# Optimization experiments

Measured on AMD Instinct MI355X. Metric: run time of the kernel, lower is better.

## Reference

```python
import jax, jax.numpy as jnp
import numpy as np

NUM_HEADS = 12
LN_EPS = 1e-12


def setup_inputs() -> dict:
    key = jax.random.key(0)
    ks = jax.random.split(key, 18)
    B, S, H, I, P, KW = 8, 128, 768, 3072, 50, 100
    s = 0.02
    inp = {
        'hidden_state': jax.random.normal(ks[0], (B, S, H), jnp.float32),
        'positive_keywords': jax.random.normal(ks[1], (P, H), jnp.float32),
        'negative_keywords': jax.random.normal(ks[2], (P, H), jnp.float32),
        'attention_mask': jnp.zeros((B, 1, 1, S), jnp.float32),
        # Bilinear weights: out = (x @ W) * keyword
        'Wq': jax.random.normal(ks[3], (H, H), jnp.float32) * s,
        'Wk': jax.random.normal(ks[4], (H, H), jnp.float32) * s,
        'Wv': jax.random.normal(ks[5], (H, H), jnp.float32) * s,
        'Wo': jax.random.normal(ks[6], (H, H), jnp.float32) * s,
        'bo': jnp.zeros((H,), jnp.float32),
        # mlp: Linear(kwcount, 1)
        'Wmlp': jax.random.normal(ks[7], (KW,), jnp.float32) * s,
        'bmlp': jnp.zeros((), jnp.float32),
        # Bottleneck FFN
        'Wdown': jax.random.normal(ks[8], (H, I), jnp.float32) * s,
        'bdown': jnp.zeros((I,), jnp.float32),
        'Wup': jax.random.normal(ks[9], (I, H), jnp.float32) * s,
        'bup': jnp.zeros((H,), jnp.float32),
        'gamma': jnp.ones((H,), jnp.float32),
        'beta': jnp.zeros((H,), jnp.float32),
    }
    return inp


def reference(hidden_state, positive_keywords, negative_keywords, attention_mask,
              Wq, Wk, Wv, Wo, bo, Wmlp, bmlp, Wdown, bdown, Wup, bup, gamma, beta):
    B, S, H = hidden_state.shape
    nh = NUM_HEADS
    hd = H // nh
    # interleave pos/neg keywords -> pool [KW, H] (diff == 0, no padding)
    pool = jnp.stack((positive_keywords, negative_keywords), axis=1).reshape(-1, H)

    # shared sequence projections (keyword modulates elementwise afterwards)
    PQ = hidden_state @ Wq  # [B,S,H]
    PK = hidden_state @ Wk
    PV = hidden_state @ Wv
    scale = 1.0 / jnp.sqrt(jnp.float32(hd))

    def per_kw(kw):  # kw: [H]
        def heads(P):
            return (P * kw).reshape(B, S, nh, hd).transpose(0, 2, 1, 3)  # [B,nh,S,hd]
        Q, K, V = heads(PQ), heads(PK), heads(PV)
        scores = jnp.einsum('bhqd,bhkd->bhqk', Q, K) * scale + attention_mask
        # NOTE: softmax over dim=-2 (query axis), faithful to the original
        w = jax.nn.softmax(scores, axis=-2)
        ctx = jnp.einsum('bhqk,bhkd->bhqd', w, V)
        ctx = ctx.transpose(0, 2, 1, 3).reshape(B, S, H)
        return ctx @ Wo + bo  # [B,S,H]

    stacked = jax.vmap(per_kw)(pool)  # [KW,B,S,H]
    # mlp Linear(KW,1) over the stacked keyword axis
    fused = jnp.einsum('kbsh,k->bsh', stacked, Wmlp) + bmlp  # [B,S,H]

    # Bottleneck FFN + residual LayerNorm (dropout = identity in eval)
    down = jax.nn.gelu(fused @ Wdown + bdown, approximate=False)
    up = down @ Wup + bup
    x = up + fused
    mu = jnp.mean(x, axis=-1, keepdims=True)
    var = jnp.var(x, axis=-1, keepdims=True)
    return gamma * (x - mu) / jnp.sqrt(var + LN_EPS) + beta
```

## Files before the change

### kernel.cpp

```cpp
#include <hip/hip_runtime.h>
#include <hip/hip_bf16.h>
#include <math.h>

#define B_ 8
#define S_ 128
#define H_ 768
#define NH_ 12
#define HD_ 64
#define M_ 1024
#define KW_ 100
#define I_ 3072
#define QKVN 2304
#define NCHUNK 10
#define KWPER 10
#define LOG2E 1.4426950408889634f

typedef __attribute__((ext_vector_type(8))) short short8;
typedef __attribute__((ext_vector_type(8))) unsigned short ushort8;
typedef __attribute__((ext_vector_type(4))) float f32x4;

static __device__ __forceinline__ unsigned short f2b(float f) {
  union { float f; unsigned int u; } v; v.f = f;
  return (unsigned short)((v.u + 0x7fffu + ((v.u >> 16) & 1u)) >> 16);
}
static __device__ __forceinline__ float b2f(unsigned short b) {
  union { unsigned int u; float f; } v; v.u = ((unsigned int)b) << 16;
  return v.f;
}

__global__ void k_prep(const float* __restrict__ hidden,
                       const float* __restrict__ Wq, const float* __restrict__ Wk,
                       const float* __restrict__ Wv, const float* __restrict__ Wo,
                       const float* __restrict__ Wdown, const float* __restrict__ Wup,
                       const float* __restrict__ posk, const float* __restrict__ negk,
                       const float* __restrict__ Wmlp, const float* __restrict__ bmlp,
                       const float* __restrict__ bo,
                       unsigned short* __restrict__ hb, unsigned short* __restrict__ qkvT,
                       unsigned short* __restrict__ WoT, unsigned short* __restrict__ WdownT,
                       unsigned short* __restrict__ WupT,
                       float* __restrict__ kw2s, float* __restrict__ kwm, float* __restrict__ c0) {
  __shared__ float tile[32][33];
  int z = blockIdx.z;
  int t = threadIdx.x;
  if (z == 6) {
    int n = blockIdx.y * 96 + blockIdx.x;
    if (n < 768) {
      int i = (n * 256 + t) * 4;
      float4 v = *(const float4*)&hidden[i];
      uint2 o;
      o.x = (unsigned)f2b(v.x) | ((unsigned)f2b(v.y) << 16);
      o.y = (unsigned)f2b(v.z) | ((unsigned)f2b(v.w) << 16);
      *(uint2*)&hb[i] = o;
    } else if (n < 1068) {
      int idx = (n - 768) * 256 + t;
      if (idx < KW_ * H_) {
        int j = idx / H_, d = idx - j * H_;
        float v = (j & 1) ? negk[(j >> 1) * H_ + d] : posk[(j >> 1) * H_ + d];
        kw2s[idx] = v * v * 0.125f * LOG2E;
        kwm[idx] = v * Wmlp[j];
      }
    } else if (n == 1068) {
      __shared__ float red[256];
      red[t] = (t < KW_) ? Wmlp[t] : 0.f;
      __syncthreads();
      for (int s = 128; s > 0; s >>= 1) { if (t < s) red[t] += red[t + s]; __syncthreads(); }
      float sWm = red[0];
      for (int c = t; c < H_; c += 256) c0[c] = sWm * bo[c] + bmlp[0];
    }
    return;
  }
  const float* src; unsigned short* dst; int R, C, r0, c0t;
  if (z < 4) {
    if (blockIdx.x >= 24) return;
    const float* srcs[4] = {Wq, Wk, Wv, Wo};
    src = srcs[z];
    dst = (z < 3) ? qkvT + (size_t)z * 768 * 768 : WoT;
    R = 768; C = 768; c0t = blockIdx.x * 32; r0 = blockIdx.y * 32;
  } else if (z == 4) {
    src = Wdown; dst = WdownT; R = 768; C = 3072;
    c0t = blockIdx.x * 32; r0 = blockIdx.y * 32;
  } else {
    src = Wup; dst = WupT; R = 3072; C = 768;
    c0t = blockIdx.y * 32; r0 = blockIdx.x * 32;
  }
  int tx = t & 31, ty = t >> 5;
#pragma unroll
  for (int i = 0; i < 4; i++)
    tile[ty + i * 8][tx] = src[(size_t)(r0 + ty + i * 8) * C + c0t + tx];
  __syncthreads();
#pragma unroll
  for (int i = 0; i < 4; i++)
    dst[(size_t)(c0t + ty + i * 8) * R + r0 + tx] = f2b(tile[tx][ty + i * 8]);
}

template <int EPI>
__launch_bounds__(256)
__global__ void k_gemm_bt(const unsigned short* __restrict__ A, const unsigned short* __restrict__ BT,
                          int M, int N, int K,
                          float* __restrict__ outF, unsigned short* __restrict__ outB,
                          const float* __restrict__ bias, const float* __restrict__ res) {
  __shared__ unsigned short Asm[128][56];
  __shared__ unsigned short Bsm[128][56];
  int tid = threadIdx.x;
  int lane = tid & 63, wid = tid >> 6;
  int g = lane >> 4, c16 = lane & 15;
  int wr = wid >> 1, wc = wid & 1;
  int m0 = blockIdx.y * 128, n0 = blockIdx.x * 128;
  f32x4 acc[4][4] = {};
  int r = tid >> 1, half = (tid & 1) * 16;
  const unsigned short* Ap = A + (size_t)(m0 + r) * K + half;
  const unsigned short* Bp = BT + (size_t)(n0 + r) * K + half;
  for (int kt = 0; kt < K; kt += 32) {
    __syncthreads();
    ushort8 a0 = *(const ushort8*)(Ap + kt);
    ushort8 a1 = *(const ushort8*)(Ap + kt + 8);
    ushort8 b0 = *(const ushort8*)(Bp + kt);
    ushort8 b1 = *(const ushort8*)(Bp + kt + 8);
    *(ushort8*)&Asm[r][half] = a0;  *(ushort8*)&Asm[r][half + 8] = a1;
    *(ushort8*)&Bsm[r][half] = b0;  *(ushort8*)&Bsm[r][half + 8] = b1;
    __syncthreads();
    short8 af[4], bf[4];
#pragma unroll
    for (int mi = 0; mi < 4; mi++) af[mi] = *(const short8*)&Asm[wr * 64 + mi * 16 + c16][g * 8];
#pragma unroll
    for (int ni = 0; ni < 4; ni++) bf[ni] = *(const short8*)&Bsm[wc * 64 + ni * 16 + c16][g * 8];
#pragma unroll
    for (int mi = 0; mi < 4; mi++)
#pragma unroll
      for (int ni = 0; ni < 4; ni++)
        acc[mi][ni] = __builtin_amdgcn_mfma_f32_16x16x32_bf16(af[mi], bf[ni], acc[mi][ni], 0, 0, 0);
  }
#pragma unroll
  for (int mi = 0; mi < 4; mi++)
#pragma unroll
    for (int ni = 0; ni < 4; ni++)
#pragma unroll
      for (int rr = 0; rr < 4; rr++) {
        int row = m0 + wr * 64 + mi * 16 + g * 4 + rr;
        int col = n0 + wc * 64 + ni * 16 + c16;
        float v = acc[mi][ni][rr];
        if (EPI == 0) {
          outB[(size_t)row * N + col] = f2b(v);
        } else if (EPI == 2) {
          float t = v + bias[col];
          float gl = 0.5f * t * (1.f + erff(t * 0.70710678118f));
          outB[(size_t)row * N + col] = f2b(gl);
        }
      }
}

__launch_bounds__(256)
__global__ void k_gemm_sk(const unsigned short* __restrict__ A, const unsigned short* __restrict__ BT,
                          int M, int N, int K, int ksl, float* __restrict__ pOut) {
  __shared__ unsigned short Asm[128][56];
  __shared__ unsigned short Bsm[128][56];
  int tid = threadIdx.x;
  int lane = tid & 63, wid = tid >> 6;
  int g = lane >> 4, c16 = lane & 15;
  int wr = wid >> 1, wc = wid & 1;
  int m0 = blockIdx.y * 128, n0 = blockIdx.x * 128;
  int kstart = blockIdx.z * ksl;
  f32x4 acc[4][4] = {};
  int r = tid >> 1, half = (tid & 1) * 16;
  const unsigned short* Ap = A + (size_t)(m0 + r) * K + half + kstart;
  const unsigned short* Bp = BT + (size_t)(n0 + r) * K + half + kstart;
  for (int kt = 0; kt < ksl; kt += 32) {
    __syncthreads();
    ushort8 a0 = *(const ushort8*)(Ap + kt);
    ushort8 a1 = *(const ushort8*)(Ap + kt + 8);
    ushort8 b0 = *(const ushort8*)(Bp + kt);
    ushort8 b1 = *(const ushort8*)(Bp + kt + 8);
    *(ushort8*)&Asm[r][half] = a0;  *(ushort8*)&Asm[r][half + 8] = a1;
    *(ushort8*)&Bsm[r][half] = b0;  *(ushort8*)&Bsm[r][half + 8] = b1;
    __syncthreads();
    short8 af[4], bf[4];
#pragma unroll
    for (int mi = 0; mi < 4; mi++) af[mi] = *(const short8*)&Asm[wr * 64 + mi * 16 + c16][g * 8];
#pragma unroll
    for (int ni = 0; ni < 4; ni++) bf[ni] = *(const short8*)&Bsm[wc * 64 + ni * 16 + c16][g * 8];
#pragma unroll
    for (int mi = 0; mi < 4; mi++)
#pragma unroll
      for (int ni = 0; ni < 4; ni++)
        acc[mi][ni] = __builtin_amdgcn_mfma_f32_16x16x32_bf16(af[mi], bf[ni], acc[mi][ni], 0, 0, 0);
  }
  float* dst = pOut + (size_t)blockIdx.z * M * N;
#pragma unroll
  for (int mi = 0; mi < 4; mi++)
#pragma unroll
    for (int ni = 0; ni < 4; ni++)
#pragma unroll
      for (int rr = 0; rr < 4; rr++) {
        int row = m0 + wr * 64 + mi * 16 + g * 4 + rr;
        int col = n0 + wc * 64 + ni * 16 + c16;
        dst[(size_t)row * N + col] = acc[mi][ni][rr];
      }
}

template <int SPLITS, int EPI>
__global__ void k_red(const float* __restrict__ p, const float* __restrict__ bias,
                      float* __restrict__ outF, unsigned short* __restrict__ outB, int N) {
  int i = (blockIdx.x * 256 + threadIdx.x) * 4;
  const size_t MN = (size_t)M_ * N;
  float4 s = *(const float4*)&p[i];
#pragma unroll
  for (int c = 1; c < SPLITS; c++) {
    float4 v = *(const float4*)&p[c * MN + i];
    s.x += v.x; s.y += v.y; s.z += v.z; s.w += v.w;
  }
  if (EPI == 1) {
    int col = i % N;
    s.x += bias[col]; s.y += bias[col + 1]; s.z += bias[col + 2]; s.w += bias[col + 3];
    *(float4*)&outF[i] = s;
  }
  uint2 o;
  o.x = (unsigned)f2b(s.x) | ((unsigned)f2b(s.y) << 16);
  o.y = (unsigned)f2b(s.z) | ((unsigned)f2b(s.w) << 16);
  *(uint2*)&outB[i] = o;
}


static __device__ __forceinline__ int swzA(int r, int c) {
  return (((r << 7) + (c << 1)) ^ ((r & 7) << 4)) >> 1;
}

__launch_bounds__(512, 2)
__global__ void k_attn(const unsigned short* __restrict__ PQKV,
                       const float* __restrict__ kw2s, const float* __restrict__ kwm,
                       float* __restrict__ partial) {
  __shared__ unsigned short Ks[128 * 64];
  __shared__ unsigned short PVT[64][136];
  __shared__ unsigned short WL[8][16 * 128];
  __shared__ float SUMS[8][128];
  __shared__ float RINV[128];
  __shared__ float kw2L[KWPER * 64];
  __shared__ float kwmL[KWPER * 64];
  int tid = threadIdx.x;
  int lane = tid & 63, wid = tid >> 6;
  int g = lane >> 4, c16 = lane & 15;
  int chunk = blockIdx.x, h = blockIdx.y, b = blockIdx.z;
  const size_t rowbase = (size_t)b * 128 * QKVN;
  int kq = tid >> 2, quarter = tid & 3;
  {
    const unsigned short* srck = PQKV + rowbase + (size_t)kq * QKVN + H_ + h * HD_ + quarter * 16;
    ushort8 v0 = *(const ushort8*)srck;
    ushort8 v1 = *(const ushort8*)(srck + 8);
    *(ushort8*)&Ks[swzA(kq, quarter * 16)] = v0;
    *(ushort8*)&Ks[swzA(kq, quarter * 16 + 8)] = v1;
    const unsigned short* srcv = PQKV + rowbase + (size_t)kq * QKVN + 2 * H_ + h * HD_ + quarter * 16;
    ushort8 w0 = *(const ushort8*)srcv;
    ushort8 w1 = *(const ushort8*)(srcv + 8);
#pragma unroll
    for (int j = 0; j < 8; j++) PVT[quarter * 16 + j][kq] = w0[j];
#pragma unroll
    for (int j = 0; j < 8; j++) PVT[quarter * 16 + 8 + j][kq] = w1[j];
    for (int i = tid; i < KWPER * 64; i += 512) {
      int ki = i >> 6, d = i & 63;
      size_t gi = (size_t)(chunk * KWPER + ki) * H_ + h * HD_ + d;
      kw2L[i] = kw2s[gi];
      kwmL[i] = kwm[gi];
    }
  }
  const unsigned short* qp = PQKV + rowbase + (size_t)(wid * 16 + c16) * QKVN + h * HD_;
  ushort8 qf0 = *(const ushort8*)(qp + g * 8);
  ushort8 qf1 = *(const ushort8*)(qp + 32 + g * 8);
  __syncthreads();
  short8 kf[8][2];
#pragma unroll
  for (int t = 0; t < 8; t++)
#pragma unroll
    for (int s = 0; s < 2; s++)
      kf[t][s] = *(const short8*)&Ks[swzA(t * 16 + c16, s * 32 + g * 8)];
  short8 vf[4][4];
#pragma unroll
  for (int dt = 0; dt < 4; dt++)
#pragma unroll
    for (int s = 0; s < 4; s++)
      vf[dt][s] = *(const short8*)&PVT[dt * 16 + c16][s * 32 + g * 8];
  char* wbuf = (char*)&WL[wid][0];
  float accO[4][4] = {};
  for (int ki = 0; ki < KWPER; ki++) {
    const float* kp = &kw2L[ki * 64];
    short8 aA0, aA1;
    {
      float4 ka = *(const float4*)&kp[g * 8];
      float4 kb = *(const float4*)&kp[g * 8 + 4];
      float4 kc = *(const float4*)&kp[32 + g * 8];
      float4 kd = *(const float4*)&kp[32 + g * 8 + 4];
      union { unsigned u[4]; short8 v; } p0, p1;
      asm("v_cvt_pk_bf16_f32 %0, %1, %2" : "=v"(p0.u[0]) : "v"(b2f(qf0[0]) * ka.x), "v"(b2f(qf0[1]) * ka.y));
      asm("v_cvt_pk_bf16_f32 %0, %1, %2" : "=v"(p0.u[1]) : "v"(b2f(qf0[2]) * ka.z), "v"(b2f(qf0[3]) * ka.w));
      asm("v_cvt_pk_bf16_f32 %0, %1, %2" : "=v"(p0.u[2]) : "v"(b2f(qf0[4]) * kb.x), "v"(b2f(qf0[5]) * kb.y));
      asm("v_cvt_pk_bf16_f32 %0, %1, %2" : "=v"(p0.u[3]) : "v"(b2f(qf0[6]) * kb.z), "v"(b2f(qf0[7]) * kb.w));
      asm("v_cvt_pk_bf16_f32 %0, %1, %2" : "=v"(p1.u[0]) : "v"(b2f(qf1[0]) * kc.x), "v"(b2f(qf1[1]) * kc.y));
      asm("v_cvt_pk_bf16_f32 %0, %1, %2" : "=v"(p1.u[1]) : "v"(b2f(qf1[2]) * kc.z), "v"(b2f(qf1[3]) * kc.w));
      asm("v_cvt_pk_bf16_f32 %0, %1, %2" : "=v"(p1.u[2]) : "v"(b2f(qf1[4]) * kd.x), "v"(b2f(qf1[5]) * kd.y));
      asm("v_cvt_pk_bf16_f32 %0, %1, %2" : "=v"(p1.u[3]) : "v"(b2f(qf1[6]) * kd.z), "v"(b2f(qf1[7]) * kd.w));
      aA0 = p0.v; aA1 = p1.v;
    }
    unsigned e[8][2];
    float s8v[8];
    __builtin_amdgcn_s_setprio(1);
#pragma unroll
    for (int t = 0; t < 8; t++) {
      f32x4 z = {0.f, 0.f, 0.f, 0.f};
      z = __builtin_amdgcn_mfma_f32_16x16x32_bf16(aA0, kf[t][0], z, 0, 0, 0);
      z = __builtin_amdgcn_mfma_f32_16x16x32_bf16(aA1, kf[t][1], z, 0, 0, 0);
      float e0 = __builtin_amdgcn_exp2f(z[0]);
      float e1 = __builtin_amdgcn_exp2f(z[1]);
      float e2 = __builtin_amdgcn_exp2f(z[2]);
      float e3 = __builtin_amdgcn_exp2f(z[3]);
      s8v[t] = (e0 + e1) + (e2 + e3);
      asm("v_cvt_pk_bf16_f32 %0, %1, %2" : "=v"(e[t][0]) : "v"(e0), "v"(e1));
      asm("v_cvt_pk_bf16_f32 %0, %1, %2" : "=v"(e[t][1]) : "v"(e2), "v"(e3));
    }
    __builtin_amdgcn_s_setprio(0);
#pragma unroll
    for (int t = 0; t < 8; t++) {
      s8v[t] += __shfl_xor(s8v[t], 16);
      s8v[t] += __shfl_xor(s8v[t], 32);
    }
    if (g == 0) {
#pragma unroll
      for (int t = 0; t < 8; t++) SUMS[wid][c16 + 16 * t] = s8v[t];
    }
    __syncthreads();
    if (tid < 128) {
      float tot = 0.f;
#pragma unroll
      for (int w = 0; w < 8; w++) tot += SUMS[w][tid];
      RINV[tid] = 1.0f / tot;
    }
    __syncthreads();
    {
      int cb2 = c16 * 2;
      int qb = g * 4;
      int xb = (g & 1) * 4;
#pragma unroll
      for (int t = 0; t < 8; t++) {
        float ri = RINV[c16 + 16 * t];
        float w0 = b2f((unsigned short)(e[t][0] & 0xffffu)) * ri;
        float w1 = b2f((unsigned short)(e[t][0] >> 16)) * ri;
        float w2 = b2f((unsigned short)(e[t][1] & 0xffffu)) * ri;
        float w3 = b2f((unsigned short)(e[t][1] >> 16)) * ri;
        unsigned p01, p23;
        asm("v_cvt_pk_bf16_f32 %0, %1, %2" : "=v"(p01) : "v"(w0), "v"(w1));
        asm("v_cvt_pk_bf16_f32 %0, %1, %2" : "=v"(p23) : "v"(w2), "v"(w3));
        int tb = t * 32 + cb2;
        int a0 = ((qb + 0) * 256 + tb) ^ ((xb + 0) << 4);
        int a1 = ((qb + 1) * 256 + tb) ^ ((xb + 1) << 4);
        int a2 = ((qb + 2) * 256 + tb) ^ ((xb + 2) << 4);
        int a3 = ((qb + 3) * 256 + tb) ^ ((xb + 3) << 4);
        *(unsigned short*)(wbuf + a0) = (unsigned short)(p01 & 0xffffu);
        *(unsigned short*)(wbuf + a1) = (unsigned short)(p01 >> 16);
        *(unsigned short*)(wbuf + a2) = (unsigned short)(p23 & 0xffffu);
        *(unsigned short*)(wbuf + a3) = (unsigned short)(p23 >> 16);
      }
    }
    short8 wf[4];
#pragma unroll
    for (int s = 0; s < 4; s++)
      wf[s] = *(const short8*)(wbuf + ((c16 * 256 + s * 64 + g * 16) ^ ((c16 & 7) << 4)));
    __builtin_amdgcn_s_setprio(1);
    f32x4 zz[4];
#pragma unroll
    for (int dt = 0; dt < 4; dt++) {
      f32x4 z = {0.f, 0.f, 0.f, 0.f};
#pragma unroll
      for (int s = 0; s < 4; s++)
        z = __builtin_amdgcn_mfma_f32_16x16x32_bf16(wf[s], vf[dt][s], z, 0, 0, 0);
      zz[dt] = z;
    }
    __builtin_amdgcn_s_setprio(0);
#pragma unroll
    for (int dt = 0; dt < 4; dt++) {
      float km = kwmL[ki * 64 + dt * 16 + c16];
#pragma unroll
      for (int rr = 0; rr < 4; rr++) accO[dt][rr] += zz[dt][rr] * km;
    }
  }
  float* dst = partial + (size_t)chunk * M_ * H_;
#pragma unroll
  for (int dt = 0; dt < 4; dt++)
#pragma unroll
    for (int rr = 0; rr < 4; rr++) {
      int q = wid * 16 + g * 4 + rr;
      dst[(size_t)(b * 128 + q) * H_ + h * HD_ + dt * 16 + c16] = accO[dt][rr];
    }
}

__global__ void k_reduce(const float* __restrict__ partial, unsigned short* __restrict__ ctxsum) {
  int i = (blockIdx.x * 256 + threadIdx.x) * 4;
  float4 s = *(const float4*)&partial[i];
#pragma unroll
  for (int c = 1; c < NCHUNK; c++) {
    float4 v = *(const float4*)&partial[(size_t)c * M_ * H_ + i];
    s.x += v.x; s.y += v.y; s.z += v.z; s.w += v.w;
  }
  uint2 o;
  o.x = (unsigned)f2b(s.x) | ((unsigned)f2b(s.y) << 16);
  o.y = (unsigned)f2b(s.z) | ((unsigned)f2b(s.w) << 16);
  *(uint2*)&ctxsum[i] = o;
}

__launch_bounds__(256)
__global__ void k_ln2(const float* __restrict__ pUp, const float* __restrict__ bup,
                      const float* __restrict__ fusedF,
                      const float* __restrict__ gamma, const float* __restrict__ beta,
                      float* __restrict__ out) {
  __shared__ float red[8];
  int row = blockIdx.x, t = threadIdx.x;
  int lane = t & 63, wid = t >> 6;
  const size_t MN = (size_t)M_ * H_;
  const size_t rb = (size_t)row * H_;
  float v[3];
#pragma unroll
  for (int j = 0; j < 3; j++) {
    int c = t + j * 256;
    float x = pUp[rb + c] + pUp[MN + rb + c] + pUp[2 * MN + rb + c] + pUp[3 * MN + rb + c];
    v[j] = x + bup[c] + fusedF[rb + c];
  }
  float s = v[0] + v[1] + v[2];
#pragma unroll
  for (int off = 1; off < 64; off <<= 1) s += __shfl_xor(s, off);
  if (lane == 0) red[wid] = s;
  __syncthreads();
  float mu = (red[0] + red[1] + red[2] + red[3]) * (1.f / 768.f);
  float q = 0.f;
#pragma unroll
  for (int j = 0; j < 3; j++) { float d = v[j] - mu; q += d * d; }
#pragma unroll
  for (int off = 1; off < 64; off <<= 1) q += __shfl_xor(q, off);
  if (lane == 0) red[4 + wid] = q;
  __syncthreads();
  float var = (red[4] + red[5] + red[6] + red[7]) * (1.f / 768.f);
  float rstd = rsqrtf(var + 1e-12f);
#pragma unroll
  for (int j = 0; j < 3; j++) {
    int c = t + j * 256;
    out[rb + c] = gamma[c] * ((v[j] - mu) * rstd) + beta[c];
  }
}


extern "C" void kernel_launch(void* const* d_in, const int* in_sizes, int n_in,
                              void* d_out, int out_size, void* d_ws, size_t ws_size,
                              hipStream_t stream) {
  const float* hidden = (const float*)d_in[0];
  const float* posk   = (const float*)d_in[1];
  const float* negk   = (const float*)d_in[2];
  const float* Wq     = (const float*)d_in[4];
  const float* Wk     = (const float*)d_in[5];
  const float* Wv     = (const float*)d_in[6];
  const float* Wo     = (const float*)d_in[7];
  const float* bo     = (const float*)d_in[8];
  const float* Wmlp   = (const float*)d_in[9];
  const float* bmlp   = (const float*)d_in[10];
  const float* Wdown  = (const float*)d_in[11];
  const float* bdown  = (const float*)d_in[12];
  const float* Wup    = (const float*)d_in[13];
  const float* bup    = (const float*)d_in[14];
  const float* gamma  = (const float*)d_in[15];
  const float* beta   = (const float*)d_in[16];

  char* ws = (char*)d_ws;
  size_t off = 0;
  auto alloc = [&](size_t bytes) -> void* {
    void* p = ws + off;
    off += (bytes + 255) & ~(size_t)255;
    return p;
  };
  unsigned short* hb     = (unsigned short*)alloc((size_t)M_ * H_ * 2);
  unsigned short* qkvT   = (unsigned short*)alloc((size_t)QKVN * H_ * 2);
  unsigned short* WoT    = (unsigned short*)alloc((size_t)H_ * H_ * 2);
  unsigned short* WdownT = (unsigned short*)alloc((size_t)I_ * H_ * 2);
  unsigned short* WupT   = (unsigned short*)alloc((size_t)H_ * I_ * 2);
  unsigned short* PQKV   = (unsigned short*)alloc((size_t)M_ * QKVN * 2);
  float* kw2s    = (float*)alloc((size_t)KW_ * H_ * 4);
  float* kwm     = (float*)alloc((size_t)KW_ * H_ * 4);
  float* c0      = (float*)alloc((size_t)H_ * 4);
  float* partial = (float*)alloc((size_t)NCHUNK * M_ * H_ * 4);
  unsigned short* ctxsum = (unsigned short*)alloc((size_t)M_ * H_ * 2);
  float* fusedF  = (float*)alloc((size_t)M_ * H_ * 4);
  unsigned short* fusedB = (unsigned short*)alloc((size_t)M_ * H_ * 2);
  unsigned short* downB  = (unsigned short*)alloc((size_t)M_ * I_ * 2);

  k_prep<<<dim3(96, 24, 7), 256, 0, stream>>>(hidden, Wq, Wk, Wv, Wo, Wdown, Wup,
                                              posk, negk, Wmlp, bmlp, bo,
                                              hb, qkvT, WoT, WdownT, WupT, kw2s, kwm, c0);
  k_gemm_sk<<<dim3(18, 8, 2), 256, 0, stream>>>(hb, qkvT, M_, QKVN, H_, 384, partial);
  k_red<2, 0><<<2304, 256, 0, stream>>>(partial, nullptr, nullptr, PQKV, QKVN);
  k_attn<<<dim3(NCHUNK, NH_, B_), 512, 0, stream>>>(PQKV, kw2s, kwm, partial);
  k_reduce<<<768, 256, 0, stream>>>(partial, ctxsum);
  k_gemm_sk<<<dim3(6, 8, 2), 256, 0, stream>>>(ctxsum, WoT, M_, H_, H_, 384, partial);
  k_red<2, 1><<<768, 256, 0, stream>>>(partial, c0, fusedF, fusedB, H_);
  k_gemm_bt<2><<<dim3(24, 8), 256, 0, stream>>>(fusedB, WdownT, M_, I_, H_, nullptr, downB, bdown, nullptr);
  k_gemm_sk<<<dim3(6, 8, 4), 256, 0, stream>>>(downB, WupT, M_, H_, I_, 768, partial);
  k_ln2<<<M_, 256, 0, stream>>>(partial, bup, fusedF, gamma, beta, (float*)d_out);
}
```

Before: 207.6 us.

## Alias attention LDS buffers, store bf16 partials, raise occupancy and split-K

```diff
diff --git a/kernel.cpp b/kernel.cpp
--- a/kernel.cpp
+++ b/kernel.cpp
@@ -224,13 +224,11 @@
   return (((r << 7) + (c << 1)) ^ ((r & 7) << 4)) >> 1;
 }
 
-__launch_bounds__(512, 2)
+__launch_bounds__(512, 6)
 __global__ void k_attn(const unsigned short* __restrict__ PQKV,
                        const float* __restrict__ kw2s, const float* __restrict__ kwm,
-                       float* __restrict__ partial) {
-  __shared__ unsigned short Ks[128 * 64];
-  __shared__ unsigned short PVT[64][136];
-  __shared__ unsigned short WL[8][16 * 128];
+                       unsigned short* __restrict__ partial) {
+  __shared__ char SM[32768];
   __shared__ float SUMS[8][128];
   __shared__ float RINV[128];
   __shared__ float kw2L[KWPER * 64];
@@ -241,19 +239,13 @@
   int chunk = blockIdx.x, h = blockIdx.y, b = blockIdx.z;
   const size_t rowbase = (size_t)b * 128 * QKVN;
   int kq = tid >> 2, quarter = tid & 3;
+  unsigned short* KsS = (unsigned short*)SM;
   {
     const unsigned short* srck = PQKV + rowbase + (size_t)kq * QKVN + H_ + h * HD_ + quarter * 16;
     ushort8 v0 = *(const ushort8*)srck;
     ushort8 v1 = *(const ushort8*)(srck + 8);
-    *(ushort8*)&Ks[swzA(kq, quarter * 16)] = v0;
-    *(ushort8*)&Ks[swzA(kq, quarter * 16 + 8)] = v1;
-    const unsigned short* srcv = PQKV + rowbase + (size_t)kq * QKVN + 2 * H_ + h * HD_ + quarter * 16;
-    ushort8 w0 = *(const ushort8*)srcv;
-    ushort8 w1 = *(const ushort8*)(srcv + 8);
-#pragma unroll
-    for (int j = 0; j < 8; j++) PVT[quarter * 16 + j][kq] = w0[j];
-#pragma unroll
-    for (int j = 0; j < 8; j++) PVT[quarter * 16 + 8 + j][kq] = w1[j];
+    *(ushort8*)&KsS[swzA(kq, quarter * 16)] = v0;
+    *(ushort8*)&KsS[swzA(kq, quarter * 16 + 8)] = v1;
     for (int i = tid; i < KWPER * 64; i += 512) {
       int ki = i >> 6, d = i & 63;
       size_t gi = (size_t)(chunk * KWPER + ki) * H_ + h * HD_ + d;
@@ -270,14 +262,30 @@
   for (int t = 0; t < 8; t++)
 #pragma unroll
     for (int s = 0; s < 2; s++)
-      kf[t][s] = *(const short8*)&Ks[swzA(t * 16 + c16, s * 32 + g * 8)];
+      kf[t][s] = *(const short8*)&KsS[swzA(t * 16 + c16, s * 32 + g * 8)];
+  __syncthreads();
+  {
+    unsigned short (*PVT)[136] = (unsigned short(*)[136])SM;
+    const unsigned short* srcv = PQKV + rowbase + (size_t)kq * QKVN + 2 * H_ + h * HD_ + quarter * 16;
+    ushort8 w0 = *(const ushort8*)srcv;
+    ushort8 w1 = *(const ushort8*)(srcv + 8);
+#pragma unroll
+    for (int j = 0; j < 8; j++) PVT[quarter * 16 + j][kq] = w0[j];
+#pragma unroll
+    for (int j = 0; j < 8; j++) PVT[quarter * 16 + 8 + j][kq] = w1[j];
+  }
+  __syncthreads();
   short8 vf[4][4];
-#pragma unroll
-  for (int dt = 0; dt < 4; dt++)
-#pragma unroll
-    for (int s = 0; s < 4; s++)
-      vf[dt][s] = *(const short8*)&PVT[dt * 16 + c16][s * 32 + g * 8];
-  char* wbuf = (char*)&WL[wid][0];
+  {
+    unsigned short (*PVT)[136] = (unsigned short(*)[136])SM;
+#pragma unroll
+    for (int dt = 0; dt < 4; dt++)
+#pragma unroll
+      for (int s = 0; s < 4; s++)
+        vf[dt][s] = *(const short8*)&PVT[dt * 16 + c16][s * 32 + g * 8];
+  }
+  __syncthreads();
+  char* wbuf = SM + wid * 4096;
   float accO[4][4] = {};
   for (int ki = 0; ki < KWPER; ki++) {
     const float* kp = &kw2L[ki * 64];
@@ -298,31 +306,29 @@
       asm("v_cvt_pk_bf16_f32 %0, %1, %2" : "=v"(p1.u[3]) : "v"(b2f(qf1[6]) * kd.z), "v"(b2f(qf1[7]) * kd.w));
       aA0 = p0.v; aA1 = p1.v;
     }
-    unsigned e[8][2];
-    float s8v[8];
+    f32x4 sc[8];
     __builtin_amdgcn_s_setprio(1);
 #pragma unroll
     for (int t = 0; t < 8; t++) {
       f32x4 z = {0.f, 0.f, 0.f, 0.f};
       z = __builtin_amdgcn_mfma_f32_16x16x32_bf16(aA0, kf[t][0], z, 0, 0, 0);
       z = __builtin_amdgcn_mfma_f32_16x16x32_bf16(aA1, kf[t][1], z, 0, 0, 0);
-      float e0 = __builtin_amdgcn_exp2f(z[0]);
-      float e1 = __builtin_amdgcn_exp2f(z[1]);
-      float e2 = __builtin_amdgcn_exp2f(z[2]);
-      float e3 = __builtin_amdgcn_exp2f(z[3]);
-      s8v[t] = (e0 + e1) + (e2 + e3);
-      asm("v_cvt_pk_bf16_f32 %0, %1, %2" : "=v"(e[t][0]) : "v"(e0), "v"(e1));
-      asm("v_cvt_pk_bf16_f32 %0, %1, %2" : "=v"(e[t][1]) : "v"(e2), "v"(e3));
+      sc[t][0] = __builtin_amdgcn_exp2f(z[0]);
+      sc[t][1] = __builtin_amdgcn_exp2f(z[1]);
+      sc[t][2] = __builtin_amdgcn_exp2f(z[2]);
+      sc[t][3] = __builtin_amdgcn_exp2f(z[3]);
     }
     __builtin_amdgcn_s_setprio(0);
+    float s8v[8];
 #pragma unroll
     for (int t = 0; t < 8; t++) {
+      s8v[t] = (sc[t][0] + sc[t][1]) + (sc[t][2] + sc[t][3]);
       s8v[t] += __shfl_xor(s8v[t], 16);
       s8v[t] += __shfl_xor(s8v[t], 32);
     }
     if (g == 0) {
 #pragma unroll
-      for (int t = 0; t < 8; t++) SUMS[wid][c16 + 16 * t] = s8v[t];
+      for (int t = 0; t < 8; t++) SUMS[wid][t * 16 + c16] = s8v[t];
     }
     __syncthreads();
     if (tid < 128) {
@@ -338,11 +344,9 @@
       int xb = (g & 1) * 4;
 #pragma unroll
       for (int t = 0; t < 8; t++) {
-        float ri = RINV[c16 + 16 * t];
-        float w0 = b2f((unsigned short)(e[t][0] & 0xffffu)) * ri;
-        float w1 = b2f((unsigned short)(e[t][0] >> 16)) * ri;
-        float w2 = b2f((unsigned short)(e[t][1] & 0xffffu)) * ri;
-        float w3 = b2f((unsigned short)(e[t][1] >> 16)) * ri;
+        float ri = RINV[t * 16 + c16];
+        float w0 = sc[t][0] * ri, w1 = sc[t][1] * ri;
+        float w2 = sc[t][2] * ri, w3 = sc[t][3] * ri;
         unsigned p01, p23;
         asm("v_cvt_pk_bf16_f32 %0, %1, %2" : "=v"(p01) : "v"(w0), "v"(w1));
         asm("v_cvt_pk_bf16_f32 %0, %1, %2" : "=v"(p23) : "v"(w2), "v"(w3));
@@ -379,27 +383,30 @@
       for (int rr = 0; rr < 4; rr++) accO[dt][rr] += zz[dt][rr] * km;
     }
   }
-  float* dst = partial + (size_t)chunk * M_ * H_;
+  unsigned short* dst = partial + (size_t)chunk * M_ * H_;
 #pragma unroll
   for (int dt = 0; dt < 4; dt++)
 #pragma unroll
     for (int rr = 0; rr < 4; rr++) {
       int q = wid * 16 + g * 4 + rr;
-      dst[(size_t)(b * 128 + q) * H_ + h * HD_ + dt * 16 + c16] = accO[dt][rr];
-    }
-}
-
-__global__ void k_reduce(const float* __restrict__ partial, unsigned short* __restrict__ ctxsum) {
+      dst[(size_t)(b * 128 + q) * H_ + h * HD_ + dt * 16 + c16] = f2b(accO[dt][rr]);
+    }
+}
+
+__global__ void k_reduce(const unsigned short* __restrict__ partial, unsigned short* __restrict__ ctxsum) {
   int i = (blockIdx.x * 256 + threadIdx.x) * 4;
-  float4 s = *(const float4*)&partial[i];
-#pragma unroll
-  for (int c = 1; c < NCHUNK; c++) {
-    float4 v = *(const float4*)&partial[(size_t)c * M_ * H_ + i];
-    s.x += v.x; s.y += v.y; s.z += v.z; s.w += v.w;
+  float s0 = 0.f, s1 = 0.f, s2 = 0.f, s3 = 0.f;
+#pragma unroll
+  for (int c = 0; c < NCHUNK; c++) {
+    uint2 v = *(const uint2*)&partial[(size_t)c * M_ * H_ + i];
+    s0 += b2f((unsigned short)(v.x & 0xffffu));
+    s1 += b2f((unsigned short)(v.x >> 16));
+    s2 += b2f((unsigned short)(v.y & 0xffffu));
+    s3 += b2f((unsigned short)(v.y >> 16));
   }
   uint2 o;
-  o.x = (unsigned)f2b(s.x) | ((unsigned)f2b(s.y) << 16);
-  o.y = (unsigned)f2b(s.z) | ((unsigned)f2b(s.w) << 16);
+  o.x = (unsigned)f2b(s0) | ((unsigned)f2b(s1) << 16);
+  o.y = (unsigned)f2b(s2) | ((unsigned)f2b(s3) << 16);
   *(uint2*)&ctxsum[i] = o;
 }
 
@@ -490,10 +497,10 @@
                                               hb, qkvT, WoT, WdownT, WupT, kw2s, kwm, c0);
   k_gemm_sk<<<dim3(18, 8, 2), 256, 0, stream>>>(hb, qkvT, M_, QKVN, H_, 384, partial);
   k_red<2, 0><<<2304, 256, 0, stream>>>(partial, nullptr, nullptr, PQKV, QKVN);
-  k_attn<<<dim3(NCHUNK, NH_, B_), 512, 0, stream>>>(PQKV, kw2s, kwm, partial);
-  k_reduce<<<768, 256, 0, stream>>>(partial, ctxsum);
-  k_gemm_sk<<<dim3(6, 8, 2), 256, 0, stream>>>(ctxsum, WoT, M_, H_, H_, 384, partial);
-  k_red<2, 1><<<768, 256, 0, stream>>>(partial, c0, fusedF, fusedB, H_);
+  k_attn<<<dim3(NCHUNK, NH_, B_), 512, 0, stream>>>(PQKV, kw2s, kwm, (unsigned short*)partial);
+  k_reduce<<<768, 256, 0, stream>>>((const unsigned short*)partial, ctxsum);
+  k_gemm_sk<<<dim3(6, 8, 4), 256, 0, stream>>>(ctxsum, WoT, M_, H_, H_, 192, partial);
+  k_red<4, 1><<<768, 256, 0, stream>>>(partial, c0, fusedF, fusedB, H_);
   k_gemm_bt<2><<<dim3(24, 8), 256, 0, stream>>>(fusedB, WdownT, M_, I_, H_, nullptr, downB, bdown, nullptr);
   k_gemm_sk<<<dim3(6, 8, 4), 256, 0, stream>>>(downB, WupT, M_, H_, I_, 768, partial);
   k_ln2<<<M_, 256, 0, stream>>>(partial, bup, fusedF, gamma, beta, (float*)d_out);
```

New measurement: 815.3 us. 293% more time.
